# Performance work log

Hardware: AMD Instinct MI355X
Metric: run time of the kernel (lower is better)

## Reference

```python
import jax, jax.numpy as jnp
import numpy as np

TEMP = 0.1
GROUPS = 16
EPS = 1e-5
COS_EPS = 1e-8


def _encoder(x, conv_w, conv_b, gn_g, gn_b):
    # Conv2d(C,C,3,pad=1) -> GroupNorm(16,C) -> ReLU -> AdaptiveAvgPool2d(1) -> Flatten
    y = jax.lax.conv_general_dilated(
        x, conv_w, window_strides=(1, 1), padding='SAME',
        dimension_numbers=('NCHW', 'OIHW', 'NCHW')) + conv_b[None, :, None, None]
    B, C, H, W = y.shape
    yg = y.reshape(B, GROUPS, C // GROUPS, H, W)
    mu = yg.mean(axis=(2, 3, 4), keepdims=True)
    var = yg.var(axis=(2, 3, 4), keepdims=True)
    yn = ((yg - mu) * jax.lax.rsqrt(var + EPS)).reshape(B, C, H, W)
    y = yn * gn_g[None, :, None, None] + gn_b[None, :, None, None]
    y = jax.nn.relu(y)
    return y.mean(axis=(2, 3))  # [B, C]


def _projector(h, w1, b1, w2, b2, ln_g, ln_b):
    h = jax.nn.relu(h @ w1 + b1)
    h = h @ w2 + b2
    mu = h.mean(axis=-1, keepdims=True)
    var = h.var(axis=-1, keepdims=True)
    return (h - mu) * jax.lax.rsqrt(var + EPS) * ln_g + ln_b


def _predictor(z, w1, b1, w2, b2):
    return jax.nn.relu(z @ w1 + b1) @ w2 + b2


def _l2norm(z):
    n = jnp.sqrt(jnp.sum(z * z, axis=1, keepdims=True))
    return z / jnp.maximum(n, COS_EPS)


def _pair_loss(zi, zj, off_idx):
    # vectorized version of the nested-loop cosine-sim + cross-entropy (label 0)
    S = (_l2norm(zi) @ _l2norm(zj).T) / TEMP  # [B, B]
    pos = jnp.diagonal(S)                     # sim(i_k, j_k)
    neg = jnp.take_along_axis(S, off_idx, axis=1)  # [B, B-1], row k = S[k, l!=k]
    logits = jnp.concatenate([pos[:, None], neg], axis=1)
    return jnp.mean(jax.nn.logsumexp(logits, axis=1) - logits[:, 0])


def setup_inputs() -> dict:
    key = jax.random.key(0)
    ks = jax.random.split(key, 32)
    B, C, H, W, P = 256, 256, 16, 16, 128
    d = {}
    d['x_t2w'] = jax.random.normal(ks[0], (B, C, H, W), jnp.float32)
    d['x_t2f'] = jax.random.normal(ks[1], (B, C, H, W), jnp.float32)
    d['x_t1n'] = jax.random.normal(ks[2], (B, C, H, W), jnp.float32)
    i = 3
    for m in ('t2w', 't2f', 't1n'):
        d[f'conv_w_{m}'] = jax.random.normal(ks[i], (C, C, 3, 3), jnp.float32) * 0.02; i += 1
        d[f'conv_b_{m}'] = jnp.zeros((C,), jnp.float32)
        d[f'gn_g_{m}'] = jnp.ones((C,), jnp.float32)
        d[f'gn_b_{m}'] = jnp.zeros((C,), jnp.float32)
    d['proj_w1'] = jax.random.normal(ks[i], (C, C), jnp.float32) * 0.02; i += 1
    d['proj_b1'] = jnp.zeros((C,), jnp.float32)
    d['proj_w2'] = jax.random.normal(ks[i], (C, P), jnp.float32) * 0.02; i += 1
    d['proj_b2'] = jnp.zeros((P,), jnp.float32)
    d['ln_g'] = jnp.ones((P,), jnp.float32)
    d['ln_b'] = jnp.zeros((P,), jnp.float32)
    d['pred_w1'] = jax.random.normal(ks[i], (P, P), jnp.float32) * 0.02; i += 1
    d['pred_b1'] = jnp.zeros((P,), jnp.float32)
    d['pred_w2'] = jax.random.normal(ks[i], (P, P), jnp.float32) * 0.02; i += 1
    d['pred_b2'] = jnp.zeros((P,), jnp.float32)
    return d


def reference(x_t2w, x_t2f, x_t1n,
              conv_w_t2w, conv_b_t2w, gn_g_t2w, gn_b_t2w,
              conv_w_t2f, conv_b_t2f, gn_g_t2f, gn_b_t2f,
              conv_w_t1n, conv_b_t1n, gn_g_t1n, gn_b_t1n,
              proj_w1, proj_b1, proj_w2, proj_b2, ln_g, ln_b,
              pred_w1, pred_b1, pred_w2, pred_b2):
    xs = [x_t2w, x_t2f, x_t1n]
    enc_params = [(conv_w_t2w, conv_b_t2w, gn_g_t2w, gn_b_t2w),
                  (conv_w_t2f, conv_b_t2f, gn_g_t2f, gn_b_t2f),
                  (conv_w_t1n, conv_b_t1n, gn_g_t1n, gn_b_t1n)]
    encoded = [_encoder(x, *p) for x, p in zip(xs, enc_params)]
    projected = [_projector(e, proj_w1, proj_b1, proj_w2, proj_b2, ln_g, ln_b) for e in encoded]
    preds = [_predictor(z, pred_w1, pred_b1, pred_w2, pred_b2) for z in projected]

    B = projected[0].shape[0]
    off_idx = jnp.asarray(np.array([[l for l in range(B) if l != k] for k in range(B)],
                                    dtype=np.int32))
    pairs = [(0, 1), (0, 2), (1, 2)]
    loss = sum(_pair_loss(projected[i], projected[j], off_idx) for i, j in pairs) / len(pairs)

    return (jnp.stack(encoded), jnp.stack(projected), jnp.stack(preds), loss)
```

## Files before the change

kernel.cpp:

```cpp
#include <hip/hip_runtime.h>
#include <hip/hip_bf16.h>

typedef float f32x4 __attribute__((ext_vector_type(4)));
typedef __bf16 bf16x8 __attribute__((ext_vector_type(8)));
typedef unsigned short u16x8 __attribute__((ext_vector_type(8)));

#define GN_EPS 1e-5f
#define LN_EPS 1e-5f
#define COS_EPS_F 1e-8f

__device__ __forceinline__ unsigned short f2bf(float f) {
  unsigned int u = __builtin_bit_cast(unsigned int, f);
  u += 0x7fffu + ((u >> 16) & 1u);
  return (unsigned short)(u >> 16);
}

__global__ void transpose_kernel(const float* __restrict__ x0,
                                 const float* __restrict__ x1,
                                 const float* __restrict__ x2,
                                 unsigned short* __restrict__ xT,
                                 unsigned int strideElems, int mBase) {
  __shared__ float lds[64][129];
  int m = mBase + (blockIdx.x >> 11);
  int bid = blockIdx.x & 2047;
  const float* x = (m == 0) ? x0 : ((m == 1) ? x1 : x2);
  unsigned short* dst = xT + (unsigned int)(m - mBase) * strideElems;

  int hwt = bid & 3, cit = (bid >> 2) & 1, b = bid >> 3;
  int hw0 = hwt * 64, ci0 = cit * 128;
  int tid = threadIdx.x;

  int hwx = tid & 63, cy0 = tid >> 6;
  const float* xb = x + (b * 256 + ci0) * 256 + hw0;
  #pragma unroll 8
  for (int p = 0; p < 32; ++p) {
    int cy = cy0 + 4 * p;
    lds[hwx][cy] = xb[cy * 256 + hwx];
  }
  __syncthreads();

  int cp = tid & 63, hy0 = tid >> 6;
  unsigned int* outp = (unsigned int*)(dst + (b * 256 + hw0) * 256 + ci0);
  #pragma unroll 4
  for (int p = 0; p < 16; ++p) {
    int hy = hy0 + 4 * p;
    float lo = lds[hy][2 * cp];
    float hi = lds[hy][2 * cp + 1];
    unsigned int w = ((unsigned int)f2bf(hi) << 16) | f2bf(lo);
    outp[hy * 128 + cp] = w;
  }
}

__global__ void pack_kernel(const float* __restrict__ w0,
                            const float* __restrict__ w1,
                            const float* __restrict__ w2,
                            unsigned short* __restrict__ wp,
                            unsigned short* __restrict__ zerobuf) {
  int m = blockIdx.y;
  const float* w = (m == 0) ? w0 : ((m == 1) ? w1 : w2);
  int idx = blockIdx.x * 256 + threadIdx.x;
  if (m == 0 && blockIdx.x == 0 && threadIdx.x < 256) zerobuf[threadIdx.x] = 0;
  int ci = idx & 255;
  int rest = idx >> 8;
  int khw = rest % 9, co = rest / 9;
  wp[m * 589824 + idx] = f2bf(w[(co * 256 + ci) * 9 + khw]);
}

__device__ __forceinline__ void gl_lds16(const unsigned short* g, unsigned short* l) {
  __builtin_amdgcn_global_load_lds(
      (const __attribute__((address_space(1))) void*)g,
      (__attribute__((address_space(3))) void*)l, 16, 0, 0);
}

__launch_bounds__(512, 2)
__global__ void conv_gn_pool(const unsigned short* __restrict__ xT,
                             unsigned int xTstride,
                             const unsigned short* __restrict__ wp,
                             const unsigned short* __restrict__ zb,
                             const float* __restrict__ cb0, const float* __restrict__ cb1,
                             const float* __restrict__ cb2,
                             const float* __restrict__ gg0, const float* __restrict__ gg1,
                             const float* __restrict__ gg2,
                             const float* __restrict__ gb0, const float* __restrict__ gb1,
                             const float* __restrict__ gb2,
                             float* __restrict__ enc, int mBase) {
  __shared__ unsigned short Ab[4][8192];
  __shared__ unsigned short Bb[4][8192];
  __shared__ float gsum[16], gsq[16], pooled[256];

  int mm = mBase + (blockIdx.x >> 8);
  int bb = blockIdx.x & 255;
  int b = (bb & 7) * 32 + (bb >> 3);
  const float* cbias = (mm == 0) ? cb0 : ((mm == 1) ? cb1 : cb2);
  const float* gng   = (mm == 0) ? gg0 : ((mm == 1) ? gg1 : gg2);
  const float* gnb   = (mm == 0) ? gb0 : ((mm == 1) ? gb1 : gb2);

  int tid = threadIdx.x;
  int wid = tid >> 6, lane = tid & 63;
  int wr = wid >> 2, wc = wid & 3;
  int l15 = lane & 15, l4 = lane >> 4;

  if (tid < 16) { gsum[tid] = 0.f; gsq[tid] = 0.f; }
  if (tid < 256) pooled[tid] = 0.f;

  int s0 = tid, s1 = 512 + tid;
  int r0 = s0 >> 2, c0 = s0 & 3;
  int r1 = s1 >> 2, c1 = s1 & 3;
  int cs0 = (c0 ^ ((r0 >> 1) & 3)) * 8;
  int cs1 = (c1 ^ ((r1 >> 1) & 3)) * 8;
  int rh0 = r0 >> 4, rw0 = r0 & 15;
  int rh1 = r1 >> 4, rw1 = r1 & 15;

  const unsigned short* xb = xT + (unsigned int)(mm - mBase) * xTstride + b * 65536;
  const unsigned short* wpm = wp + mm * 589824;
  const unsigned short* bB0 = wpm + r0 * 2304 + cs0;
  const unsigned short* bB1 = wpm + r1 * 2304 + cs1;

  int kch = (l4 ^ ((l15 >> 1) & 3)) * 8;
  int base_af = (wr * 128 + l15) * 32 + kch;
  int base_bf = (wc * 64 + l15) * 32 + kch;

  f32x4 acc[8][4];
  #pragma unroll
  for (int i = 0; i < 8; ++i)
    #pragma unroll
    for (int j = 0; j < 4; ++j) acc[i][j] = (f32x4)(0.0f);

  int kc3 = 0, kh3 = 0, kw3 = 0;

  #define STAGE(SBUF)                                                          \
    {                                                                          \
      int ci0_ = kc3 * 32;                                                     \
      unsigned short* dstA = &Ab[(SBUF)][0];                                   \
      int h0_ = rh0 + kh3 - 1, w0_ = rw0 + kw3 - 1;                            \
      const unsigned short* sA0 = ((unsigned)h0_ < 16u && (unsigned)w0_ < 16u) \
          ? xb + ((h0_ * 16 + w0_) * 256 + ci0_ + cs0) : zb;                   \
      gl_lds16(sA0, dstA + s0 * 8);                                            \
      int h1_ = rh1 + kh3 - 1, w1_ = rw1 + kw3 - 1;                            \
      const unsigned short* sA1 = ((unsigned)h1_ < 16u && (unsigned)w1_ < 16u) \
          ? xb + ((h1_ * 16 + w1_) * 256 + ci0_ + cs1) : zb;                   \
      gl_lds16(sA1, dstA + s1 * 8);                                            \
      int offB = (kh3 * 3 + kw3) * 256 + ci0_;                                 \
      unsigned short* dstB = &Bb[(SBUF)][0];                                   \
      gl_lds16(bB0 + offB, dstB + s0 * 8);                                     \
      gl_lds16(bB1 + offB, dstB + s1 * 8);                                     \
      kw3 = kw3 + 1; int cw_ = (kw3 == 3); kw3 = cw_ ? 0 : kw3; kh3 += cw_;    \
      int ch_ = (kh3 == 3); kh3 = ch_ ? 0 : kh3; kc3 += ch_;                   \
    }

  #define LD8(P) __builtin_bit_cast(bf16x8, *(const u16x8*)(P))

  bf16x8 afA_P[4], afA_Q[4], bfr_P[4], bfr_Q[4], afB[4];

  #define TILE_BODY(BUF, BUF1, SBUF, CUR, NXT, DO_STAGE, VMN, DO_NEXT)         \
    {                                                                          \
      asm volatile("s_waitcnt vmcnt(" #VMN ")" ::: "memory");                  \
      __builtin_amdgcn_s_barrier();                                            \
      if (DO_STAGE) STAGE(SBUF);                                               \
      const unsigned short* Ap = &Ab[(BUF)][0];                                \
      _Pragma("unroll")                                                        \
      for (int j = 0; j < 4; ++j)                                              \
        afB[j] = LD8(&Ap[base_af + (4 + j) * 512]);                            \
      if (DO_NEXT) {                                                           \
        const unsigned short* Ap1 = &Ab[(BUF1)][0];                            \
        const unsigned short* Bp1 = &Bb[(BUF1)][0];                            \
        _Pragma("unroll")                                                      \
        for (int n = 0; n < 4; ++n)                                            \
          bfr_##NXT[n] = LD8(&Bp1[base_bf + n * 512]);                         \
        _Pragma("unroll")                                                      \
        for (int j = 0; j < 4; ++j)                                            \
          afA_##NXT[j] = LD8(&Ap1[base_af + j * 512]);                         \
      }                                                                        \
      __builtin_amdgcn_sched_barrier(0);                                       \
      __builtin_amdgcn_s_setprio(1);                                           \
      _Pragma("unroll")                                                        \
      for (int j = 0; j < 4; ++j)                                              \
        _Pragma("unroll")                                                      \
        for (int n = 0; n < 4; ++n)                                            \
          acc[j][n] = __builtin_amdgcn_mfma_f32_16x16x32_bf16(                 \
              afA_##CUR[j], bfr_##CUR[n], acc[j][n], 0, 0, 0);                 \
      _Pragma("unroll")                                                        \
      for (int j = 0; j < 4; ++j)                                              \
        _Pragma("unroll")                                                      \
        for (int n = 0; n < 4; ++n)                                            \
          acc[4 + j][n] = __builtin_amdgcn_mfma_f32_16x16x32_bf16(             \
              afB[j], bfr_##CUR[n], acc[4 + j][n], 0, 0, 0);                   \
      __builtin_amdgcn_s_setprio(0);                                           \
    }

  STAGE(0); STAGE(1); STAGE(2);
  asm volatile("s_waitcnt vmcnt(8)" ::: "memory");
  __builtin_amdgcn_s_barrier();
  {
    const unsigned short* Ap0 = &Ab[0][0];
    const unsigned short* Bp0 = &Bb[0][0];
    #pragma unroll
    for (int n = 0; n < 4; ++n) bfr_P[n] = LD8(&Bp0[base_bf + n * 512]);
    #pragma unroll
    for (int j = 0; j < 4; ++j) afA_P[j] = LD8(&Ap0[base_af + j * 512]);
  }

  for (int it = 0; it < 17; ++it) {
    TILE_BODY(0, 1, 3, P, Q, 1, 4, 1);
    TILE_BODY(1, 2, 0, Q, P, 1, 4, 1);
    TILE_BODY(2, 3, 1, P, Q, 1, 4, 1);
    TILE_BODY(3, 0, 2, Q, P, 1, 4, 1);
  }
  TILE_BODY(0, 1, 3, P, Q, 1, 4, 1);
  TILE_BODY(1, 2, 0, Q, P, 0, 4, 1);
  TILE_BODY(2, 3, 1, P, Q, 0, 0, 1);
  TILE_BODY(3, 0, 2, Q, P, 0, 0, 0);
  #undef TILE_BODY
  #undef STAGE
  #undef LD8

  __syncthreads();

  float bias[4], ggv[4], gbv[4];
  #pragma unroll
  for (int nf = 0; nf < 4; ++nf) {
    int co = wc * 64 + nf * 16 + l15;
    bias[nf] = cbias[co]; ggv[nf] = gng[co]; gbv[nf] = gnb[co];
  }
  #pragma unroll
  for (int nf = 0; nf < 4; ++nf) {
    float s1 = 0.f, s2 = 0.f;
    #pragma unroll
    for (int mf = 0; mf < 8; ++mf)
      #pragma unroll
      for (int i = 0; i < 4; ++i) {
        float v = acc[mf][nf][i] + bias[nf];
        acc[mf][nf][i] = v;
        s1 += v; s2 += v * v;
      }
    #pragma unroll
    for (int d = 1; d < 64; d <<= 1) {
      s1 += __shfl_xor(s1, d);
      s2 += __shfl_xor(s2, d);
    }
    if (lane == 0) {
      atomicAdd(&gsum[wc * 4 + nf], s1);
      atomicAdd(&gsq[wc * 4 + nf], s2);
    }
  }
  __syncthreads();
  #pragma unroll
  for (int nf = 0; nf < 4; ++nf) {
    int g = wc * 4 + nf;
    float mean = gsum[g] * (1.f / 4096.f);
    float var = gsq[g] * (1.f / 4096.f) - mean * mean;
    float rs = rsqrtf(var + GN_EPS);
    float p = 0.f;
    #pragma unroll
    for (int mf = 0; mf < 8; ++mf)
      #pragma unroll
      for (int i = 0; i < 4; ++i) {
        float v = (acc[mf][nf][i] - mean) * rs * ggv[nf] + gbv[nf];
        p += fmaxf(v, 0.f);
      }
    p += __shfl_xor(p, 16);
    p += __shfl_xor(p, 32);
    if (lane < 16) atomicAdd(&pooled[wc * 64 + nf * 16 + l15], p);
  }
  __syncthreads();
  if (tid < 256)
    enc[mm * 65536 + b * 256 + tid] = pooled[tid] * (1.f / 256.f);
}

__global__ void proj_pred(const float* __restrict__ enc,
                          const float* __restrict__ w1, const float* __restrict__ b1,
                          const float* __restrict__ w2, const float* __restrict__ b2,
                          const float* __restrict__ lng, const float* __restrict__ lnb,
                          const float* __restrict__ pw1, const float* __restrict__ pb1,
                          const float* __restrict__ pw2, const float* __restrict__ pb2,
                          float* __restrict__ proj, float* __restrict__ pred,
                          float* __restrict__ znorm) {
  __shared__ float row[256], h1[256], zz[128], p1[128], red[2];
  int r = blockIdx.x, tid = threadIdx.x;
  row[tid] = enc[r * 256 + tid];
  __syncthreads();
  float a = 0.f;
  for (int k = 0; k < 256; ++k) a += row[k] * w1[k * 256 + tid];
  h1[tid] = fmaxf(a + b1[tid], 0.f);
  __syncthreads();
  if (tid < 128) {
    a = 0.f;
    for (int k = 0; k < 256; ++k) a += h1[k] * w2[k * 128 + tid];
    zz[tid] = a + b2[tid];
  }
  __syncthreads();
  if (tid == 0) {
    float m = 0.f;
    for (int k = 0; k < 128; ++k) m += zz[k];
    m *= (1.f / 128.f);
    float v = 0.f;
    for (int k = 0; k < 128; ++k) { float d = zz[k] - m; v += d * d; }
    red[0] = m;
    red[1] = rsqrtf(v * (1.f / 128.f) + LN_EPS);
  }
  __syncthreads();
  float zval = 0.f;
  if (tid < 128) {
    zval = (zz[tid] - red[0]) * red[1] * lng[tid] + lnb[tid];
    proj[r * 128 + tid] = zval;
  }
  __syncthreads();
  if (tid < 128) zz[tid] = zval;
  __syncthreads();
  if (tid == 0) {
    float s = 0.f;
    for (int k = 0; k < 128; ++k) s += zz[k] * zz[k];
    red[0] = 1.f / fmaxf(sqrtf(s), COS_EPS_F);
  }
  __syncthreads();
  if (tid < 128) {
    znorm[r * 128 + tid] = zz[tid] * red[0];
    a = 0.f;
    for (int k = 0; k < 128; ++k) a += zz[k] * pw1[k * 128 + tid];
    p1[tid] = fmaxf(a + pb1[tid], 0.f);
  }
  __syncthreads();
  if (tid < 128) {
    a = 0.f;
    for (int k = 0; k < 128; ++k) a += p1[k] * pw2[k * 128 + tid];
    pred[r * 128 + tid] = a + pb2[tid];
  }
}

__global__ void loss_kernel(const float* __restrict__ zn, float* __restrict__ part) {
  __shared__ float zi[128], sv[256], rbuf[256];
  int blk = blockIdx.x;
  int p = blk >> 8, k = blk & 255;
  int i = (p == 2) ? 1 : 0;
  int j = (p == 0) ? 1 : 2;
  int tid = threadIdx.x;
  if (tid < 128) zi[tid] = zn[(i * 256 + k) * 128 + tid];
  __syncthreads();
  const float4* zj = (const float4*)&zn[(j * 256 + tid) * 128];
  float s = 0.f;
  #pragma unroll 8
  for (int d = 0; d < 32; ++d) {
    float4 aq = *(const float4*)&zi[d * 4];
    float4 bq = zj[d];
    s += aq.x * bq.x + aq.y * bq.y + aq.z * bq.z + aq.w * bq.w;
  }
  s *= 10.0f;
  sv[tid] = s;
  rbuf[tid] = s;
  __syncthreads();
  for (int d = 128; d > 0; d >>= 1) {
    if (tid < d) rbuf[tid] = fmaxf(rbuf[tid], rbuf[tid + d]);
    __syncthreads();
  }
  float m = rbuf[0];
  __syncthreads();
  rbuf[tid] = expf(s - m);
  __syncthreads();
  for (int d = 128; d > 0; d >>= 1) {
    if (tid < d) rbuf[tid] += rbuf[tid + d];
    __syncthreads();
  }
  if (tid == 0) part[blk] = m + logf(rbuf[0]) - sv[k];
}

__global__ void finalize_loss(const float* __restrict__ part, float* __restrict__ out) {
  __shared__ float red[256];
  int tid = threadIdx.x;
  float s = 0.f;
  for (int idx = tid; idx < 768; idx += 256) s += part[idx];
  red[tid] = s;
  __syncthreads();
  for (int d = 128; d > 0; d >>= 1) {
    if (tid < d) red[tid] += red[tid + d];
    __syncthreads();
  }
  if (tid == 0) out[0] = red[0] * (1.f / 768.f);
}

extern "C" void kernel_launch(void* const* d_in, const int* in_sizes, int n_in,
                              void* d_out, int out_size, void* d_ws, size_t ws_size,
                              hipStream_t stream) {
  const float* x[3]  = {(const float*)d_in[0], (const float*)d_in[1], (const float*)d_in[2]};
  const float* cw[3] = {(const float*)d_in[3], (const float*)d_in[7], (const float*)d_in[11]};
  const float* cb[3] = {(const float*)d_in[4], (const float*)d_in[8], (const float*)d_in[12]};
  const float* gg[3] = {(const float*)d_in[5], (const float*)d_in[9], (const float*)d_in[13]};
  const float* gb[3] = {(const float*)d_in[6], (const float*)d_in[10], (const float*)d_in[14]};
  const float* p_w1 = (const float*)d_in[15];
  const float* p_b1 = (const float*)d_in[16];
  const float* p_w2 = (const float*)d_in[17];
  const float* p_b2 = (const float*)d_in[18];
  const float* ln_g = (const float*)d_in[19];
  const float* ln_b = (const float*)d_in[20];
  const float* q_w1 = (const float*)d_in[21];
  const float* q_b1 = (const float*)d_in[22];
  const float* q_w2 = (const float*)d_in[23];
  const float* q_b2 = (const float*)d_in[24];

  float* out = (float*)d_out;
  char* ws = (char*)d_ws;

  const size_t XT_ONE = 33554432;
  bool merged = ws_size >= (3 * XT_ONE + 3538944 + 393216 + 3072 + 512);

  size_t xt_total = merged ? 3 * XT_ONE : XT_ONE;
  unsigned short* xT  = (unsigned short*)ws;
  unsigned short* wpk = (unsigned short*)(ws + xt_total);
  float* znorm = (float*)(ws + xt_total + 3538944);
  float* part  = (float*)(ws + xt_total + 3538944 + 393216);
  unsigned short* zb = (unsigned short*)(ws + xt_total + 3538944 + 393216 + 3072);

  float* enc  = out;
  float* proj = out + 196608;
  float* pred = out + 294912;
  float* lossp = out + 393216;

  pack_kernel<<<dim3(2304, 3), dim3(256), 0, stream>>>(cw[0], cw[1], cw[2], wpk, zb);

  if (merged) {
    transpose_kernel<<<dim3(6144), dim3(256), 0, stream>>>(x[0], x[1], x[2], xT, 16777216u, 0);
    conv_gn_pool<<<dim3(768), dim3(512), 0, stream>>>(
        xT, 16777216u, wpk, zb, cb[0], cb[1], cb[2], gg[0], gg[1], gg[2],
        gb[0], gb[1], gb[2], enc, 0);
  } else {
    for (int m = 0; m < 3; ++m) {
      transpose_kernel<<<dim3(2048), dim3(256), 0, stream>>>(x[0], x[1], x[2], xT, 0u, m);
      conv_gn_pool<<<dim3(256), dim3(512), 0, stream>>>(
          xT, 0u, wpk, zb, cb[0], cb[1], cb[2], gg[0], gg[1], gg[2],
          gb[0], gb[1], gb[2], enc, m);
    }
  }
  proj_pred<<<dim3(768), dim3(256), 0, stream>>>(enc, p_w1, p_b1, p_w2, p_b2, ln_g, ln_b,
                                                 q_w1, q_b1, q_w2, q_b2, proj, pred, znorm);
  loss_kernel<<<dim3(768), dim3(256), 0, stream>>>(znorm, part);
  finalize_loss<<<dim3(1), dim3(256), 0, stream>>>(part, lossp);
}
```

Baseline: 323.0 us.

## Restructure conv MFMA pipeline to ping-pong fragment loads and tree-reduce LayerNorm

The conv main loop is rewritten from a three-stage-ahead, half-prefetched fragment scheme into a two-stage-ahead global-to-LDS pipeline. All A and B fragments for the next tile are read into alternating register sets, and a partial lgkmcnt wait lets MFMAs start before every LDS read has landed. This is meant to overlap LDS reads with MFMA work more fully, at the cost of a shallower global prefetch and more live fragment registers. Separately, the serial single-thread LayerNorm and L2-norm reductions in proj_pred are replaced with shared-memory tree reductions.

```diff
diff --git a/kernel.cpp b/kernel.cpp
--- a/kernel.cpp
+++ b/kernel.cpp
@@ -59,7 +59,7 @@
   int m = blockIdx.y;
   const float* w = (m == 0) ? w0 : ((m == 1) ? w1 : w2);
   int idx = blockIdx.x * 256 + threadIdx.x;
-  if (m == 0 && blockIdx.x == 0 && threadIdx.x < 256) zerobuf[threadIdx.x] = 0;
+  if (m == 0 && blockIdx.x == 0) zerobuf[threadIdx.x] = 0;
   int ci = idx & 255;
   int rest = idx >> 8;
   int khw = rest % 9, co = rest / 9;
@@ -150,67 +150,68 @@
 
   #define LD8(P) __builtin_bit_cast(bf16x8, *(const u16x8*)(P))
 
-  bf16x8 afA_P[4], afA_Q[4], bfr_P[4], bfr_Q[4], afB[4];
-
-  #define TILE_BODY(BUF, BUF1, SBUF, CUR, NXT, DO_STAGE, VMN, DO_NEXT)         \
+  bf16x8 afP[8], bfrP[4], afQ[8], bfrQ[4];
+
+  #define READF(AF, BF, BUFI)                                                  \
     {                                                                          \
-      asm volatile("s_waitcnt vmcnt(" #VMN ")" ::: "memory");                  \
-      __builtin_amdgcn_s_barrier();                                            \
-      if (DO_STAGE) STAGE(SBUF);                                               \
-      const unsigned short* Ap = &Ab[(BUF)][0];                                \
+      const unsigned short* Ap_ = &Ab[(BUFI)][0];                              \
+      const unsigned short* Bp_ = &Bb[(BUFI)][0];                              \
       _Pragma("unroll")                                                        \
-      for (int j = 0; j < 4; ++j)                                              \
-        afB[j] = LD8(&Ap[base_af + (4 + j) * 512]);                            \
-      if (DO_NEXT) {                                                           \
-        const unsigned short* Ap1 = &Ab[(BUF1)][0];                            \
-        const unsigned short* Bp1 = &Bb[(BUF1)][0];                            \
-        _Pragma("unroll")                                                      \
-        for (int n = 0; n < 4; ++n)                                            \
-          bfr_##NXT[n] = LD8(&Bp1[base_bf + n * 512]);                         \
-        _Pragma("unroll")                                                      \
-        for (int j = 0; j < 4; ++j)                                            \
-          afA_##NXT[j] = LD8(&Ap1[base_af + j * 512]);                         \
-      }                                                                        \
-      __builtin_amdgcn_sched_barrier(0);                                       \
+      for (int j = 0; j < 8; ++j) AF[j] = LD8(&Ap_[base_af + j * 512]);        \
+      _Pragma("unroll")                                                        \
+      for (int n = 0; n < 4; ++n) BF[n] = LD8(&Bp_[base_bf + n * 512]);        \
+    }
+
+  #define MM(AF, BF)                                                           \
+    {                                                                          \
       __builtin_amdgcn_s_setprio(1);                                           \
       _Pragma("unroll")                                                        \
-      for (int j = 0; j < 4; ++j)                                              \
+      for (int j = 0; j < 8; ++j)                                              \
         _Pragma("unroll")                                                      \
         for (int n = 0; n < 4; ++n)                                            \
           acc[j][n] = __builtin_amdgcn_mfma_f32_16x16x32_bf16(                 \
-              afA_##CUR[j], bfr_##CUR[n], acc[j][n], 0, 0, 0);                 \
-      _Pragma("unroll")                                                        \
-      for (int j = 0; j < 4; ++j)                                              \
-        _Pragma("unroll")                                                      \
-        for (int n = 0; n < 4; ++n)                                            \
-          acc[4 + j][n] = __builtin_amdgcn_mfma_f32_16x16x32_bf16(             \
-              afB[j], bfr_##CUR[n], acc[4 + j][n], 0, 0, 0);                   \
+              AF[j], BF[n], acc[j][n], 0, 0, 0);                               \
       __builtin_amdgcn_s_setprio(0);                                           \
     }
 
-  STAGE(0); STAGE(1); STAGE(2);
-  asm volatile("s_waitcnt vmcnt(8)" ::: "memory");
+  STAGE(0); STAGE(1);
+  asm volatile("s_waitcnt vmcnt(4)" ::: "memory");
   __builtin_amdgcn_s_barrier();
-  {
-    const unsigned short* Ap0 = &Ab[0][0];
-    const unsigned short* Bp0 = &Bb[0][0];
-    #pragma unroll
-    for (int n = 0; n < 4; ++n) bfr_P[n] = LD8(&Bp0[base_bf + n * 512]);
-    #pragma unroll
-    for (int j = 0; j < 4; ++j) afA_P[j] = LD8(&Ap0[base_af + j * 512]);
-  }
-
-  for (int it = 0; it < 17; ++it) {
-    TILE_BODY(0, 1, 3, P, Q, 1, 4, 1);
-    TILE_BODY(1, 2, 0, Q, P, 1, 4, 1);
-    TILE_BODY(2, 3, 1, P, Q, 1, 4, 1);
-    TILE_BODY(3, 0, 2, Q, P, 1, 4, 1);
-  }
-  TILE_BODY(0, 1, 3, P, Q, 1, 4, 1);
-  TILE_BODY(1, 2, 0, Q, P, 0, 4, 1);
-  TILE_BODY(2, 3, 1, P, Q, 0, 0, 1);
-  TILE_BODY(3, 0, 2, Q, P, 0, 0, 0);
-  #undef TILE_BODY
+  READF(afP, bfrP, 0);
+
+  for (int t2 = 0; t2 < 35; ++t2) {
+    {
+      int t = 2 * t2;
+      STAGE((t + 2) & 3);
+      asm volatile("s_waitcnt vmcnt(4)" ::: "memory");
+      __builtin_amdgcn_s_barrier();
+      READF(afQ, bfrQ, (t + 1) & 3);
+      asm volatile("s_waitcnt lgkmcnt(12)" ::: "memory");
+      __builtin_amdgcn_sched_barrier(0);
+      MM(afP, bfrP);
+    }
+    {
+      int t = 2 * t2 + 1;
+      STAGE((t + 2) & 3);
+      asm volatile("s_waitcnt vmcnt(4)" ::: "memory");
+      __builtin_amdgcn_s_barrier();
+      READF(afP, bfrP, (t + 1) & 3);
+      asm volatile("s_waitcnt lgkmcnt(12)" ::: "memory");
+      __builtin_amdgcn_sched_barrier(0);
+      MM(afQ, bfrQ);
+    }
+  }
+  asm volatile("s_waitcnt vmcnt(0)" ::: "memory");
+  __builtin_amdgcn_s_barrier();
+  READF(afQ, bfrQ, 3);
+  asm volatile("s_waitcnt lgkmcnt(12)" ::: "memory");
+  __builtin_amdgcn_sched_barrier(0);
+  MM(afP, bfrP);
+  asm volatile("s_waitcnt lgkmcnt(0)" ::: "memory");
+  __builtin_amdgcn_sched_barrier(0);
+  MM(afQ, bfrQ);
+  #undef MM
+  #undef READF
   #undef STAGE
   #undef LD8
 
@@ -275,7 +276,7 @@
                           const float* __restrict__ pw2, const float* __restrict__ pb2,
                           float* __restrict__ proj, float* __restrict__ pred,
                           float* __restrict__ znorm) {
-  __shared__ float row[256], h1[256], zz[128], p1[128], red[2];
+  __shared__ float row[256], h1[256], zz[128], p1[128], rbuf[128], red[2];
   int r = blockIdx.x, tid = threadIdx.x;
   row[tid] = enc[r * 256 + tid];
   __syncthreads();
@@ -289,32 +290,39 @@
     zz[tid] = a + b2[tid];
   }
   __syncthreads();
-  if (tid == 0) {
-    float m = 0.f;
-    for (int k = 0; k < 128; ++k) m += zz[k];
-    m *= (1.f / 128.f);
-    float v = 0.f;
-    for (int k = 0; k < 128; ++k) { float d = zz[k] - m; v += d * d; }
-    red[0] = m;
-    red[1] = rsqrtf(v * (1.f / 128.f) + LN_EPS);
-  }
+  if (tid < 128) rbuf[tid] = zz[tid];
+  __syncthreads();
+  for (int d = 64; d > 0; d >>= 1) {
+    if (tid < d) rbuf[tid] += rbuf[tid + d];
+    __syncthreads();
+  }
+  float mean = rbuf[0] * (1.f / 128.f);
+  __syncthreads();
+  if (tid < 128) { float dv = zz[tid] - mean; rbuf[tid] = dv * dv; }
+  __syncthreads();
+  for (int d = 64; d > 0; d >>= 1) {
+    if (tid < d) rbuf[tid] += rbuf[tid + d];
+    __syncthreads();
+  }
+  float rstd = rsqrtf(rbuf[0] * (1.f / 128.f) + LN_EPS);
   __syncthreads();
   float zval = 0.f;
   if (tid < 128) {
-    zval = (zz[tid] - red[0]) * red[1] * lng[tid] + lnb[tid];
+    zval = (zz[tid] - mean) * rstd * lng[tid] + lnb[tid];
     proj[r * 128 + tid] = zval;
+    rbuf[tid] = zval * zval;
   }
   __syncthreads();
   if (tid < 128) zz[tid] = zval;
-  __syncthreads();
-  if (tid == 0) {
-    float s = 0.f;
-    for (int k = 0; k < 128; ++k) s += zz[k] * zz[k];
-    red[0] = 1.f / fmaxf(sqrtf(s), COS_EPS_F);
-  }
+  for (int d = 64; d > 0; d >>= 1) {
+    __syncthreads();
+    if (tid < d) rbuf[tid] += rbuf[tid + d];
+  }
+  __syncthreads();
+  float rn = 1.f / fmaxf(sqrtf(rbuf[0]), COS_EPS_F);
   __syncthreads();
   if (tid < 128) {
-    znorm[r * 128 + tid] = zz[tid] * red[0];
+    znorm[r * 128 + tid] = zz[tid] * rn;
     a = 0.f;
     for (int k = 0; k < 128; ++k) a += zz[k] * pw1[k * 128 + tid];
     p1[tid] = fmaxf(a + pb1[tid], 0.f);
```

Result: faster. 299.8 us (-7.2%).
